# Performance work log

Measured on AMD Instinct MI355X. Metric: run time of the kernel, lower is better.

The kernel has to match this reference:

```python
import jax, jax.numpy as jnp
import numpy as np

T, B, NA = 32, 32, 5          # timesteps, envs, actions
HID, FEAT = 256, 512          # lstm hidden, cnn features
IN_DIM = FEAT + NA            # lstm input size (517)
FLAT = 64 * 7 * 7             # cnn flatten size (3136)


def _conv(x, w, b, s):
    # x: NCHW, w: OIHW, VALID padding, stride s
    y = jax.lax.conv_general_dilated(x, w, (s, s), 'VALID',
                                     dimension_numbers=('NCHW', 'OIHW', 'NCHW'))
    return y + b[None, :, None, None]


def setup_inputs() -> dict:
    key = jax.random.key(0)
    ks = jax.random.split(key, 24)
    p = lambda k, shape: (jax.random.normal(k, shape, jnp.float32) * 0.05)
    return {
        'image': jax.random.uniform(ks[0], (T * B, 3, 84, 84), jnp.float32) * 255.0,
        'last_action': jax.random.randint(ks[1], (T * B,), 0, NA),
        'done': jax.random.bernoulli(ks[2], 0.05, (T * B,)).astype(jnp.float32),
        'h0': jnp.zeros((B, HID), jnp.float32),
        'c0': jnp.zeros((B, HID), jnp.float32),
        # NatureCNN params
        'W1': p(ks[3], (32, 3, 8, 8)), 'b1': jnp.zeros((32,), jnp.float32),
        'W2': p(ks[4], (64, 32, 4, 4)), 'b2': jnp.zeros((64,), jnp.float32),
        'W3': p(ks[5], (64, 64, 3, 3)), 'b3': jnp.zeros((64,), jnp.float32),
        'Wfc': p(ks[6], (FEAT, FLAT)), 'bfc': jnp.zeros((FEAT,), jnp.float32),
        # LSTM params (torch gate order i,f,g,o)
        'W_ih': p(ks[7], (4 * HID, IN_DIM)), 'W_hh': p(ks[8], (4 * HID, HID)),
        'b_ih': jnp.zeros((4 * HID,), jnp.float32), 'b_hh': jnp.zeros((4 * HID,), jnp.float32),
        # policy MLP (hidden 64, tanh)
        'Wp1': p(ks[9], (64, HID)), 'bp1': jnp.zeros((64,), jnp.float32),
        'Wp2': p(ks[10], (NA, 64)) * 0.01, 'bp2': jnp.zeros((NA,), jnp.float32),
        # value MLP
        'Wv1': p(ks[11], (64, HID)), 'bv1': jnp.zeros((64,), jnp.float32),
        'Wv2': p(ks[12], (1, 64)), 'bv2': jnp.zeros((1,), jnp.float32),
    }


def reference(image, last_action, done, h0, c0,
              W1, b1, W2, b2, W3, b3, Wfc, bfc,
              W_ih, W_hh, b_ih, b_hh,
              Wp1, bp1, Wp2, bp2, Wv1, bv1, Wv2, bv2):
    # --- extract: NatureCNN + one-hot(last_action) ---
    x = image / 255.0
    x = jax.nn.relu(_conv(x, W1, b1, 4))   # (TB,32,20,20)
    x = jax.nn.relu(_conv(x, W2, b2, 2))   # (TB,64,9,9)
    x = jax.nn.relu(_conv(x, W3, b3, 1))   # (TB,64,7,7)
    x = x.reshape(x.shape[0], -1)
    feat = jax.nn.relu(x @ Wfc.T + bfc)    # (TB,512)
    oh = jax.nn.one_hot(last_action, NA, dtype=feat.dtype)
    xs = jnp.concatenate([feat, oh], axis=1).reshape(T, B, IN_DIM)
    ds = done.reshape(T, B)

    # --- remember: done-masked LSTM recurrence (torch gate order i,f,g,o) ---
    def step(carry, inp):
        h, c = carry
        xt, dt = inp
        m = (1.0 - dt)[:, None]
        h = h * m
        c = c * m
        g = xt @ W_ih.T + b_ih + h @ W_hh.T + b_hh   # (B, 4*HID)
        i, f, gg, o = jnp.split(g, 4, axis=1)
        c = jax.nn.sigmoid(f) * c + jax.nn.sigmoid(i) * jnp.tanh(gg)
        h = jax.nn.sigmoid(o) * jnp.tanh(c)
        return (h, c), h

    (hT, cT), hs = jax.lax.scan(step, (h0, c0), (xs, ds))
    h = hs.reshape(T * B, HID)

    # --- heads ---
    logits = jnp.tanh(h @ Wp1.T + bp1) @ Wp2.T + bp2   # (TB, NA)
    v = jnp.tanh(h @ Wv1.T + bv1) @ Wv2.T + bv2        # (TB, 1)
    return logits, v, hT, cT
```

## Files before the change

kernel.cpp:

```cpp
#include <hip/hip_runtime.h>
#include <math.h>

typedef float  f4v __attribute__((ext_vector_type(4)));
typedef short  s8v __attribute__((ext_vector_type(8)));
typedef int    i4v __attribute__((ext_vector_type(4)));

__device__ __forceinline__ float sigm(float x) { return 1.f / (1.f + expf(-x)); }
__device__ __forceinline__ unsigned short f2bf(float f) {
    unsigned int u = __float_as_uint(f);
    return (unsigned short)((u + 0x7FFF + ((u >> 16) & 1)) >> 16);
}
__device__ __forceinline__ unsigned int cvt2(float lo, float hi) {
    unsigned int r;
    asm("v_cvt_pk_bf16_f32 %0, %1, %2" : "=v"(r) : "v"(lo), "v"(hi));
    return r;
}
__device__ __forceinline__ s8v pack8(float4 a, float4 b) {
    union { unsigned int u[4]; s8v v; } r;
    r.u[0] = cvt2(a.x, a.y); r.u[1] = cvt2(a.z, a.w);
    r.u[2] = cvt2(b.x, b.y); r.u[3] = cvt2(b.z, b.w);
    return r.v;
}

__global__ __launch_bounds__(256) void k_amax(const float* __restrict__ Whh,
                                              unsigned int* __restrict__ amax_bits) {
    int i = blockIdx.x * 256 + threadIdx.x;
    float v = fabsf(Whh[i]);
#pragma unroll
    for (int o = 1; o < 64; o <<= 1) v = fmaxf(v, __shfl_xor(v, o));
    if ((threadIdx.x & 63) == 0) atomicMax(amax_bits, __float_as_uint(v));
}

__global__ __launch_bounds__(256) void k_prep(const float* __restrict__ W2, const float* __restrict__ W3,
                                              const float* __restrict__ Wfc, const float* __restrict__ Wih,
                                              const float* __restrict__ W1, const float* __restrict__ Whh,
                                              const unsigned int* __restrict__ amax_bits,
                                              unsigned short* __restrict__ W2p, unsigned short* __restrict__ W3p,
                                              unsigned short* __restrict__ Wfcp, unsigned short* __restrict__ Wihp,
                                              unsigned short* __restrict__ W1p, signed char* __restrict__ Wq) {
    int i = blockIdx.x * 256 + threadIdx.x;
    if (i < 32768) {
        int co = i >> 9, k = i & 511, t = k >> 5, ci = k & 31, ky = t >> 2, kx = t & 3;
        W2p[i] = f2bf(W2[co * 512 + ci * 16 + ky * 4 + kx]);
    } else if (i < 69632) {
        int j = i - 32768;
        int co = j / 576, k = j - co * 576, t = k >> 6, ci = k & 63;
        int ky = t / 3, kx = t - ky * 3;
        W3p[j] = f2bf(W3[((co * 64 + ci) * 3 + ky) * 3 + kx]);
    } else if (i < 1675264) {
        int j = i - 69632;
        Wfcp[j] = f2bf(Wfc[j]);
    } else if (i < 2199552) {
        int j = i - 1675264;
        int n = j >> 9, k = j & 511;
        Wihp[j] = f2bf(Wih[n * 517 + k]);
    } else if (i < 2205696) {
        int j = i - 2199552;
        W1p[j] = f2bf(W1[j] * (1.f / 255.f));
    } else if (i < 2467840) {
        int j = i - 2205696;
        float amax = __uint_as_float(amax_bits[0]);
        float s = 127.f / amax;
        int qv = (int)rintf(Whh[j] * s);
        qv = qv > 127 ? 127 : (qv < -127 ? -127 : qv);
        Wq[j] = (signed char)qv;
    }
}

__global__ __launch_bounds__(256) void k_conv1(const float* __restrict__ img,
                                               const unsigned short* __restrict__ Bw,
                                               const float* __restrict__ bias,
                                               unsigned short* __restrict__ out) {
    __shared__ unsigned short c1s[32][132];
    int lane = threadIdx.x & 63, w = threadIdx.x >> 6;
    int l15 = lane & 15, q = lane >> 4;
    int m0 = blockIdx.x * 128;
    const float* Ap[2];
#pragma unroll
    for (int mf = 0; mf < 2; ++mf) {
        int m = m0 + w * 32 + mf * 16 + l15;
        int im = m / 400, p = m - im * 400;
        int oy = p / 20, ox = p - oy * 20;
        Ap[mf] = img + im * 21168 + oy * 336 + ox * 4;
    }
    const unsigned short* Bp0 = Bw + l15 * 192 + q * 8;
    const unsigned short* Bp1 = Bw + (16 + l15) * 192 + q * 8;
    s8v bf0[6], bf1[6];
#pragma unroll
    for (int ks = 0; ks < 6; ++ks) {
        bf0[ks] = *(const s8v*)(Bp0 + ks * 32);
        bf1[ks] = *(const s8v*)(Bp1 + ks * 32);
    }
    int roffs[6];
#pragma unroll
    for (int ks = 0; ks < 6; ++ks) {
        int k0 = ks * 32 + q * 8;
        int c = k0 >> 6, ky = (k0 >> 3) & 7;
        roffs[ks] = c * 7056 + ky * 84;
    }
    f4v acc[4];
#pragma unroll
    for (int i = 0; i < 4; ++i) acc[i] = (f4v){0.f, 0.f, 0.f, 0.f};
#pragma unroll
    for (int ks = 0; ks < 6; ++ks) {
#pragma unroll
        for (int mf = 0; mf < 2; ++mf) {
            float4 a0 = *(const float4*)(Ap[mf] + roffs[ks]);
            float4 a1 = *(const float4*)(Ap[mf] + roffs[ks] + 4);
            s8v ua = pack8(a0, a1);
            acc[mf * 2 + 0] = __builtin_amdgcn_mfma_f32_16x16x32_bf16(ua, bf0[ks], acc[mf * 2 + 0], 0, 0, 0);
            acc[mf * 2 + 1] = __builtin_amdgcn_mfma_f32_16x16x32_bf16(ua, bf1[ks], acc[mf * 2 + 1], 0, 0, 0);
        }
    }
#pragma unroll
    for (int nf = 0; nf < 2; ++nf) {
        int n = nf * 16 + l15;
        float b = bias[n];
#pragma unroll
        for (int mf = 0; mf < 2; ++mf) {
            int ml = w * 32 + mf * 16 + q * 4;
#pragma unroll
            for (int r = 0; r < 4; r += 2) {
                float v0 = acc[mf * 2 + nf][r] + b;     v0 = v0 > 0.f ? v0 : 0.f;
                float v1 = acc[mf * 2 + nf][r + 1] + b; v1 = v1 > 0.f ? v1 : 0.f;
                *(unsigned int*)&c1s[n][ml + r] = cvt2(v0, v1);
            }
        }
    }
    __syncthreads();
#pragma unroll
    for (int seg = 0; seg < 16; ++seg) {
        int flat = seg * 256 + threadIdx.x;
        int n = flat >> 7, ml = flat & 127;
        int m = m0 + ml;
        int im = m / 400, p = m - im * 400;
        out[(im * 32 + n) * 400 + p] = c1s[n][ml];
    }
}

__global__ __launch_bounds__(256, 2) void k_conv2(const unsigned short* __restrict__ A,
                                                  const unsigned short* __restrict__ Bw,
                                                  const float* __restrict__ bias,
                                                  unsigned short* __restrict__ out) {
    __shared__ unsigned short sA[800 * 32];
    __shared__ unsigned short c2s[64][196];
    int tid = threadIdx.x;
    int lane = tid & 63, w = tid >> 6;
    int l15 = lane & 15, q = lane >> 4;
    int img0 = blockIdx.x * 2;
    char* sAb = (char*)sA;
    const s8v* srcv = (const s8v*)(A + img0 * 12800);
    for (int wi = tid; wi < 3200; wi += 256) {
        s8v v = srcv[wi];
        int f = wi * 8;
        int im = f / 12800, r = f - im * 12800, ci = r / 400, p = r - ci * 400;
#pragma unroll
        for (int j = 0; j < 8; ++j) {
            int R = im * 400 + p + j;
            int Rl = (R >> 1) + (R & 1) * 400;
            int by = (Rl * 32 + ci) * 2 ^ ((Rl & 7) << 4);
            *(unsigned short*)(sAb + by) = (unsigned short)v[j];
        }
    }
    __syncthreads();
    int Rb[3];
#pragma unroll
    for (int mf = 0; mf < 3; ++mf) {
        int t = w * 3 + mf;
        int im = t / 6;
        int pp = (t - im * 6) * 16 + l15;
        int px = pp > 80 ? 80 : pp;
        int oy = px / 9, ox = px - oy * 9;
        Rb[mf] = im * 400 + oy * 40 + ox * 2;
    }
    const unsigned short* Bp0 = Bw + l15 * 512 + q * 8;
    const unsigned short* Bp1 = Bw + (16 + l15) * 512 + q * 8;
    const unsigned short* Bp2 = Bw + (32 + l15) * 512 + q * 8;
    const unsigned short* Bp3 = Bw + (48 + l15) * 512 + q * 8;
    f4v acc[3][4];
#pragma unroll
    for (int i = 0; i < 3; ++i)
#pragma unroll
        for (int j = 0; j < 4; ++j) acc[i][j] = (f4v){0.f, 0.f, 0.f, 0.f};
#pragma unroll
    for (int s = 0; s < 16; ++s) {
        const int ky = s >> 2, kx = s & 3;
        const int d = ky * 20 + kx;
        s8v a[3];
#pragma unroll
        for (int mf = 0; mf < 3; ++mf) {
            int R = Rb[mf] + d;
            int Rl = (R >> 1) + (R & 1) * 400;
            int by = (Rl * 64 + q * 16) ^ ((Rl & 7) << 4);
            a[mf] = *(const s8v*)(sAb + by);
        }
        s8v b0 = *(const s8v*)(Bp0 + s * 32);
        s8v b1 = *(const s8v*)(Bp1 + s * 32);
        s8v b2 = *(const s8v*)(Bp2 + s * 32);
        s8v b3 = *(const s8v*)(Bp3 + s * 32);
#pragma unroll
        for (int mf = 0; mf < 3; ++mf) {
            acc[mf][0] = __builtin_amdgcn_mfma_f32_16x16x32_bf16(a[mf], b0, acc[mf][0], 0, 0, 0);
            acc[mf][1] = __builtin_amdgcn_mfma_f32_16x16x32_bf16(a[mf], b1, acc[mf][1], 0, 0, 0);
            acc[mf][2] = __builtin_amdgcn_mfma_f32_16x16x32_bf16(a[mf], b2, acc[mf][2], 0, 0, 0);
            acc[mf][3] = __builtin_amdgcn_mfma_f32_16x16x32_bf16(a[mf], b3, acc[mf][3], 0, 0, 0);
        }
    }
#pragma unroll
    for (int nf = 0; nf < 4; ++nf) {
        int co = nf * 16 + l15;
        float b = bias[co];
#pragma unroll
        for (int mf = 0; mf < 3; ++mf) {
            int rr = (w * 3 + mf) * 16 + q * 4;
#pragma unroll
            for (int r = 0; r < 4; r += 2) {
                float v0 = acc[mf][nf][r] + b;     v0 = v0 > 0.f ? v0 : 0.f;
                float v1 = acc[mf][nf][r + 1] + b; v1 = v1 > 0.f ? v1 : 0.f;
                *(unsigned int*)&c2s[co][rr + r] = cvt2(v0, v1);
            }
        }
    }
    __syncthreads();
    for (int idx = tid; idx < 10368; idx += 256) {
        int im = idx / 5184, r2 = idx - im * 5184, co = r2 / 81, p = r2 - co * 81;
        out[(img0 + im) * 5184 + r2] = c2s[co][im * 96 + p];
    }
}

__global__ __launch_bounds__(256, 2) void k_conv3(const unsigned short* __restrict__ A,
                                                  const unsigned short* __restrict__ Bw,
                                                  const float* __restrict__ bias,
                                                  unsigned short* __restrict__ out) {
    __shared__ unsigned short sA[162 * 64];
    __shared__ unsigned short c3s[64][132];
    int tid = threadIdx.x;
    int lane = tid & 63, w = tid >> 6;
    int l15 = lane & 15, q = lane >> 4;
    int img0 = blockIdx.x * 2;
    char* sAb = (char*)sA;
    const s8v* srcv = (const s8v*)(A + img0 * 5184);
    for (int wi = tid; wi < 1296; wi += 256) {
        s8v v = srcv[wi];
        int f = wi * 8;
#pragma unroll
        for (int j = 0; j < 8; ++j) {
            int fe = f + j;
            int im = fe / 5184, r = fe - im * 5184, ci = r / 81, p = r - ci * 81;
            int R = im * 81 + p;
            int by = (R * 64 + ci) * 2 ^ ((R & 7) << 4);
            *(unsigned short*)(sAb + by) = (unsigned short)v[j];
        }
    }
    __syncthreads();
    int Rb[2];
#pragma unroll
    for (int mf = 0; mf < 2; ++mf) {
        int t = w * 2 + mf;
        int im = t >> 2;
        int pp = (t & 3) * 16 + l15;
        int px = pp > 48 ? 48 : pp;
        int oy = px / 7, ox = px - oy * 7;
        Rb[mf] = im * 81 + oy * 9 + ox;
    }
    const unsigned short* Bp0 = Bw + l15 * 576 + q * 8;
    const unsigned short* Bp1 = Bw + (16 + l15) * 576 + q * 8;
    const unsigned short* Bp2 = Bw + (32 + l15) * 576 + q * 8;
    const unsigned short* Bp3 = Bw + (48 + l15) * 576 + q * 8;
    f4v acc[2][4];
#pragma unroll
    for (int i = 0; i < 2; ++i)
#pragma unroll
        for (int j = 0; j < 4; ++j) acc[i][j] = (f4v){0.f, 0.f, 0.f, 0.f};
#pragma unroll
    for (int s = 0; s < 18; ++s) {
        const int tap = s >> 1, cb2 = (s & 1) * 64;
        const int ky = tap / 3, kx = tap - ky * 3;
        const int d = ky * 9 + kx;
        s8v a0, a1;
        {
            int R = Rb[0] + d;
            int by = (R * 128 + cb2 + q * 16) ^ ((R & 7) << 4);
            a0 = *(const s8v*)(sAb + by);
        }
        {
            int R = Rb[1] + d;
            int by = (R * 128 + cb2 + q * 16) ^ ((R & 7) << 4);
            a1 = *(const s8v*)(sAb + by);
        }
        s8v b0 = *(const s8v*)(Bp0 + s * 32);
        s8v b1 = *(const s8v*)(Bp1 + s * 32);
        s8v b2 = *(const s8v*)(Bp2 + s * 32);
        s8v b3 = *(const s8v*)(Bp3 + s * 32);
        acc[0][0] = __builtin_amdgcn_mfma_f32_16x16x32_bf16(a0, b0, acc[0][0], 0, 0, 0);
        acc[0][1] = __builtin_amdgcn_mfma_f32_16x16x32_bf16(a0, b1, acc[0][1], 0, 0, 0);
        acc[0][2] = __builtin_amdgcn_mfma_f32_16x16x32_bf16(a0, b2, acc[0][2], 0, 0, 0);
        acc[0][3] = __builtin_amdgcn_mfma_f32_16x16x32_bf16(a0, b3, acc[0][3], 0, 0, 0);
        acc[1][0] = __builtin_amdgcn_mfma_f32_16x16x32_bf16(a1, b0, acc[1][0], 0, 0, 0);
        acc[1][1] = __builtin_amdgcn_mfma_f32_16x16x32_bf16(a1, b1, acc[1][1], 0, 0, 0);
        acc[1][2] = __builtin_amdgcn_mfma_f32_16x16x32_bf16(a1, b2, acc[1][2], 0, 0, 0);
        acc[1][3] = __builtin_amdgcn_mfma_f32_16x16x32_bf16(a1, b3, acc[1][3], 0, 0, 0);
    }
#pragma unroll
    for (int nf = 0; nf < 4; ++nf) {
        int co = nf * 16 + l15;
        float b = bias[co];
#pragma unroll
        for (int mf = 0; mf < 2; ++mf) {
            int rr = (w * 2 + mf) * 16 + q * 4;
#pragma unroll
            for (int r = 0; r < 4; r += 2) {
                float v0 = acc[mf][nf][r] + b;     v0 = v0 > 0.f ? v0 : 0.f;
                float v1 = acc[mf][nf][r + 1] + b; v1 = v1 > 0.f ? v1 : 0.f;
                *(unsigned int*)&c3s[co][rr + r] = cvt2(v0, v1);
            }
        }
    }
    __syncthreads();
    for (int idx = tid; idx < 6272; idx += 256) {
        int im = idx / 3136, r2 = idx - im * 3136, co = r2 / 49, p = r2 - co * 49;
        out[(img0 + im) * 3136 + r2] = c3s[co][im * 64 + p];
    }
}

__global__ __launch_bounds__(256) void k_fc(const unsigned short* __restrict__ A,
                                            const unsigned short* __restrict__ Bw,
                                            const float* __restrict__ bias,
                                            unsigned short* __restrict__ out) {
    int lane = threadIdx.x & 63, w = threadIdx.x >> 6;
    int l15 = lane & 15, q = lane >> 4;
    int m0 = blockIdx.x * 32 + (w & 1) * 16;
    int n0 = blockIdx.y * 64 + (w >> 1) * 32;
    const unsigned short* Ap = A + (m0 + l15) * 3136 + q * 8;
    const unsigned short* B0 = Bw + (n0 + l15) * 3136 + q * 8;
    const unsigned short* B1 = B0 + 16 * 3136;
    f4v acc0 = (f4v){0.f, 0.f, 0.f, 0.f}, acc1 = (f4v){0.f, 0.f, 0.f, 0.f};
    s8v av = *(const s8v*)Ap, b0 = *(const s8v*)B0, b1 = *(const s8v*)B1;
    for (int c = 0; c < 97; ++c) {
        Ap += 32; B0 += 32; B1 += 32;
        s8v nav = *(const s8v*)Ap, nb0 = *(const s8v*)B0, nb1 = *(const s8v*)B1;
        acc0 = __builtin_amdgcn_mfma_f32_16x16x32_bf16(av, b0, acc0, 0, 0, 0);
        acc1 = __builtin_amdgcn_mfma_f32_16x16x32_bf16(av, b1, acc1, 0, 0, 0);
        av = nav; b0 = nb0; b1 = nb1;
    }
    acc0 = __builtin_amdgcn_mfma_f32_16x16x32_bf16(av, b0, acc0, 0, 0, 0);
    acc1 = __builtin_amdgcn_mfma_f32_16x16x32_bf16(av, b1, acc1, 0, 0, 0);
    float bi0 = bias[n0 + l15], bi1 = bias[n0 + 16 + l15];
#pragma unroll
    for (int r = 0; r < 4; ++r) {
        int m = m0 + q * 4 + r;
        float v0 = acc0[r] + bi0; v0 = v0 > 0.f ? v0 : 0.f;
        float v1 = acc1[r] + bi1; v1 = v1 > 0.f ? v1 : 0.f;
        out[m * 512 + n0 + l15] = f2bf(v0);
        out[m * 512 + n0 + 16 + l15] = f2bf(v1);
    }
}

__global__ __launch_bounds__(256) void k_gx(const unsigned short* __restrict__ A,
                                            const unsigned short* __restrict__ Bw,
                                            const float* __restrict__ Wih,
                                            const float* __restrict__ bih,
                                            const float* __restrict__ bhh,
                                            const int* __restrict__ act,
                                            float* __restrict__ out) {
    int lane = threadIdx.x & 63, w = threadIdx.x >> 6;
    int l15 = lane & 15, q = lane >> 4;
    int m0 = blockIdx.x * 32 + (w & 1) * 16;
    int n0 = blockIdx.y * 64 + (w >> 1) * 32;
    const unsigned short* Ap = A + (m0 + l15) * 512 + q * 8;
    const unsigned short* B0 = Bw + (n0 + l15) * 512 + q * 8;
    const unsigned short* B1 = B0 + 16 * 512;
    f4v acc0 = (f4v){0.f, 0.f, 0.f, 0.f}, acc1 = (f4v){0.f, 0.f, 0.f, 0.f};
    for (int c = 0; c < 16; ++c) {
        s8v av = *(const s8v*)Ap;
        s8v b0 = *(const s8v*)B0;
        s8v b1 = *(const s8v*)B1;
        Ap += 32; B0 += 32; B1 += 32;
        acc0 = __builtin_amdgcn_mfma_f32_16x16x32_bf16(av, b0, acc0, 0, 0, 0);
        acc1 = __builtin_amdgcn_mfma_f32_16x16x32_bf16(av, b1, acc1, 0, 0, 0);
    }
    int na = n0 + l15, nb = n0 + 16 + l15;
    float ca = bih[na] + bhh[na], cb_ = bih[nb] + bhh[nb];
#pragma unroll
    for (int r = 0; r < 4; ++r) {
        int m = m0 + q * 4 + r;
        int a = act[m];
        out[m * 1024 + na] = acc0[r] + Wih[na * 517 + 512 + a] + ca;
        out[m * 1024 + nb] = acc1[r] + Wih[nb * 517 + 512 + a] + cb_;
    }
}

__global__ __launch_bounds__(1024) void k_lstm_all(const float* __restrict__ h0,
                                                   const float* __restrict__ c0,
                                                   const float* __restrict__ done,
                                                   const float* __restrict__ gx,
                                                   const signed char* __restrict__ Wq,
                                                   const unsigned int* __restrict__ amax_bits,
                                                   float* __restrict__ hs,
                                                   float* __restrict__ cb) {
    int b = blockIdx.x;
    int tid = threadIdx.x;
    int w = tid >> 6, lane = tid & 63;
    int l15 = lane & 15, q = lane >> 4;
    __shared__ float gbuf[1024];
    __shared__ float cst[256];
    __shared__ signed char hA[4][64][16];

    i4v wfr[4][4];
    const signed char* wb = Wq + (w * 64 + l15) * 256 + q * 16;
#pragma unroll
    for (int s = 0; s < 4; ++s)
#pragma unroll
        for (int kf = 0; kf < 4; ++kf)
            wfr[s][kf] = *(const i4v*)(wb + s * 16 * 256 + kf * 64);
    float sw = __uint_as_float(amax_bits[0]) * (1.f / (127.f * 127.f));

    ((int*)hA)[tid] = 0;
    __syncthreads();
    if (tid < 256) {
        int u = tid;
        cst[u] = c0[b * 256 + u];
        float m0v = 1.f - done[b];
        float hv = h0[b * 256 + u] * m0v;
        hv = hv > 1.f ? 1.f : (hv < -1.f ? -1.f : hv);
        hA[u >> 6][((u >> 4) & 3) * 16][u & 15] = (signed char)(int)rintf(hv * 127.f);
    }
    __syncthreads();

    for (int t = 0; t < 32; ++t) {
        float gxi = 0.f, gxf = 0.f, gxg = 0.f, gxo = 0.f, dcur = 0.f, dnxt = 0.f;
        if (tid < 256) {
            const float* gr = gx + (t * 32 + b) * 1024;
            gxi = gr[tid]; gxf = gr[256 + tid]; gxg = gr[512 + tid]; gxo = gr[768 + tid];
            dcur = done[t * 32 + b];
            dnxt = (t < 31) ? done[(t + 1) * 32 + b] : 1.f;
        }
        i4v acc[4];
#pragma unroll
        for (int s = 0; s < 4; ++s) acc[s] = (i4v){0, 0, 0, 0};
#pragma unroll
        for (int kf = 0; kf < 4; ++kf) {
            i4v a = *(const i4v*)&hA[kf][lane][0];
#pragma unroll
            for (int s = 0; s < 4; ++s)
                acc[s] = __builtin_amdgcn_mfma_i32_16x16x64_i8(a, wfr[s][kf], acc[s], 0, 0, 0);
        }
        if (q == 0) {
#pragma unroll
            for (int s = 0; s < 4; ++s)
                gbuf[w * 64 + s * 16 + l15] = (float)acc[s][0];
        }
        __syncthreads();
        if (tid < 256) {
            int u = tid;
            float gi = gbuf[u] * sw + gxi;
            float gf = gbuf[256 + u] * sw + gxf;
            float gg = gbuf[512 + u] * sw + gxg;
            float go = gbuf[768 + u] * sw + gxo;
            float cm = cst[u] * (1.f - dcur);
            float cn = sigm(gf) * cm + sigm(gi) * tanhf(gg);
            float hn = sigm(go) * tanhf(cn);
            cst[u] = cn;
            hs[t * 8192 + b * 256 + u] = hn;
            float hv = hn * (1.f - dnxt);
            hA[u >> 6][((u >> 4) & 3) * 16][u & 15] = (signed char)(int)rintf(hv * 127.f);
        }
        __syncthreads();
    }
    if (tid < 256) cb[b * 256 + tid] = cst[tid];
}

__global__ __launch_bounds__(256) void k_heads(const float* __restrict__ hs,
                                               const float* __restrict__ cb,
                                               const float* __restrict__ Wp1, const float* __restrict__ bp1,
                                               const float* __restrict__ Wp2, const float* __restrict__ bp2,
                                               const float* __restrict__ Wv1, const float* __restrict__ bv1,
                                               const float* __restrict__ Wv2, const float* __restrict__ bv2,
                                               float* __restrict__ out) {
    int lane = threadIdx.x & 63;
    int m = blockIdx.x * 4 + (threadIdx.x >> 6);
    const float4* hv = (const float4*)(hs + m * 256);
    const float4* wp = (const float4*)(Wp1 + lane * 256);
    const float4* wq = (const float4*)(Wv1 + lane * 256);
    float ap = 0.f, av = 0.f;
#pragma unroll 8
    for (int k = 0; k < 64; ++k) {
        float4 h4 = hv[k];
        float4 p4 = wp[k];
        float4 q4 = wq[k];
        ap += h4.x * p4.x + h4.y * p4.y + h4.z * p4.z + h4.w * p4.w;
        av += h4.x * q4.x + h4.y * q4.y + h4.z * q4.z + h4.w * q4.w;
    }
    float hp = tanhf(ap + bp1[lane]);
    float hq = tanhf(av + bv1[lane]);
#pragma unroll
    for (int j = 0; j < 5; ++j) {
        float s = hp * Wp2[j * 64 + lane];
        s += __shfl_xor(s, 1); s += __shfl_xor(s, 2); s += __shfl_xor(s, 4);
        s += __shfl_xor(s, 8); s += __shfl_xor(s, 16); s += __shfl_xor(s, 32);
        if (lane == 0) out[m * 5 + j] = s + bp2[j];
    }
    float s = hq * Wv2[lane];
    s += __shfl_xor(s, 1); s += __shfl_xor(s, 2); s += __shfl_xor(s, 4);
    s += __shfl_xor(s, 8); s += __shfl_xor(s, 16); s += __shfl_xor(s, 32);
    if (lane == 0) out[5120 + m] = s + bv2[0];

    int g = blockIdx.x * 256 + threadIdx.x;
    if (g < 8192) {
        out[6144 + g] = hs[31 * 8192 + g];
        out[6144 + 8192 + g] = cb[g];
    }
}

extern "C" void kernel_launch(void* const* d_in, const int* in_sizes, int n_in,
                              void* d_out, int out_size, void* d_ws, size_t ws_size,
                              hipStream_t stream) {
    const float* image = (const float*)d_in[0];
    const int*   act   = (const int*)d_in[1];
    const float* done  = (const float*)d_in[2];
    const float* h0    = (const float*)d_in[3];
    const float* c0    = (const float*)d_in[4];
    const float* W1    = (const float*)d_in[5];
    const float* b1    = (const float*)d_in[6];
    const float* W2    = (const float*)d_in[7];
    const float* b2    = (const float*)d_in[8];
    const float* W3    = (const float*)d_in[9];
    const float* b3    = (const float*)d_in[10];
    const float* Wfc   = (const float*)d_in[11];
    const float* bfc   = (const float*)d_in[12];
    const float* Wih   = (const float*)d_in[13];
    const float* Whh   = (const float*)d_in[14];
    const float* bih   = (const float*)d_in[15];
    const float* bhh   = (const float*)d_in[16];
    const float* Wp1   = (const float*)d_in[17];
    const float* bp1   = (const float*)d_in[18];
    const float* Wp2   = (const float*)d_in[19];
    const float* bp2   = (const float*)d_in[20];
    const float* Wv1   = (const float*)d_in[21];
    const float* bv1   = (const float*)d_in[22];
    const float* Wv2   = (const float*)d_in[23];
    const float* bv2   = (const float*)d_in[24];
    float* out = (float*)d_out;
    char* base = (char*)d_ws;

    unsigned short* a1   = (unsigned short*)(base);
    unsigned short* a2   = (unsigned short*)(base + 26214432);
    unsigned short* W2p  = (unsigned short*)(base + 36831328);
    unsigned short* W3p  = (unsigned short*)(base + 36896864);
    unsigned short* Wfcp = (unsigned short*)(base + 36970592);
    unsigned short* Wihp = (unsigned short*)(base + 40181856);
    unsigned short* W1p  = (unsigned short*)(base + 41230432);
    unsigned int*   amax = (unsigned int*)(base + 41242752);
    signed char*    Wq   = (signed char*)(base + 41242784);
    unsigned short* a3   = (unsigned short*)(base);
    unsigned short* feat = (unsigned short*)(base + 6422528);
    float* gx = (float*)(base + 7471104);
    float* hs = (float*)(base + 11665408);
    float* cb = (float*)(base + 12713984);

    hipMemsetAsync(amax, 0, 4, stream);
    k_amax<<<1024, 256, 0, stream>>>(Whh, amax);
    k_prep<<<9640, 256, 0, stream>>>(W2, W3, Wfc, Wih, W1, Whh, amax, W2p, W3p, Wfcp, Wihp, W1p, Wq);
    k_conv1<<<3200, 256, 0, stream>>>(image, W1p, b1, a1);
    k_conv2<<<512, 256, 0, stream>>>(a1, W2p, b2, a2);
    k_conv3<<<512, 256, 0, stream>>>(a2, W3p, b3, a3);
    k_fc<<<dim3(32, 8), 256, 0, stream>>>(a3, Wfcp, bfc, feat);
    k_gx<<<dim3(32, 16), 256, 0, stream>>>(feat, Wihp, Wih, bih, bhh, act, gx);
    k_lstm_all<<<32, 1024, 0, stream>>>(h0, c0, done, gx, Wq, amax, hs, cb);
    k_heads<<<256, 256, 0, stream>>>(hs, cb, Wp1, bp1, Wp2, bp2, Wv1, bv1, Wv2, bv2, out);
}
```

Baseline: 431.9 us.

## Stage whole image in LDS as bf16 for conv1, one block per image

conv1 now assigns one 512-thread block per image. Each block first converts the whole 3x84x84 fp32 image to bf16 in shared memory, then the MFMA A-fragments are read from LDS rather than as strided global float4 loads. Because stride-4 windows of size 8 overlap, each image pixel is now fetched from global memory about once instead of several times. The output tile reuses the same LDS buffer and is written out with coalesced 32-bit stores per image. The cost is about 42 KB of LDS per block, which limits occupancy, and only 25 of 32 wave-tile slots do work.

```diff
diff --git a/kernel.cpp b/kernel.cpp
--- a/kernel.cpp
+++ b/kernel.cpp
@@ -14,12 +14,6 @@
     unsigned int r;
     asm("v_cvt_pk_bf16_f32 %0, %1, %2" : "=v"(r) : "v"(lo), "v"(hi));
     return r;
-}
-__device__ __forceinline__ s8v pack8(float4 a, float4 b) {
-    union { unsigned int u[4]; s8v v; } r;
-    r.u[0] = cvt2(a.x, a.y); r.u[1] = cvt2(a.z, a.w);
-    r.u[2] = cvt2(b.x, b.y); r.u[3] = cvt2(b.z, b.w);
-    return r.v;
 }
 
 __global__ __launch_bounds__(256) void k_amax(const float* __restrict__ Whh,
@@ -67,22 +61,23 @@
     }
 }
 
-__global__ __launch_bounds__(256) void k_conv1(const float* __restrict__ img,
+__global__ __launch_bounds__(512) void k_conv1(const float* __restrict__ img,
                                                const unsigned short* __restrict__ Bw,
                                                const float* __restrict__ bias,
                                                unsigned short* __restrict__ out) {
-    __shared__ unsigned short c1s[32][132];
-    int lane = threadIdx.x & 63, w = threadIdx.x >> 6;
+    __shared__ unsigned short sImg[21168];
+    int tid = threadIdx.x;
+    int lane = tid & 63, w = tid >> 6;
     int l15 = lane & 15, q = lane >> 4;
-    int m0 = blockIdx.x * 128;
-    const float* Ap[2];
-#pragma unroll
-    for (int mf = 0; mf < 2; ++mf) {
-        int m = m0 + w * 32 + mf * 16 + l15;
-        int im = m / 400, p = m - im * 400;
-        int oy = p / 20, ox = p - oy * 20;
-        Ap[mf] = img + im * 21168 + oy * 336 + ox * 4;
-    }
+    int im = blockIdx.x;
+    const float4* srcv = (const float4*)(img + im * 21168);
+    unsigned int* sW = (unsigned int*)sImg;
+    for (int wi = tid; wi < 5292; wi += 512) {
+        float4 v = srcv[wi];
+        sW[wi * 2]     = cvt2(v.x, v.y);
+        sW[wi * 2 + 1] = cvt2(v.z, v.w);
+    }
+    __syncthreads();
     const unsigned short* Bp0 = Bw + l15 * 192 + q * 8;
     const unsigned short* Bp1 = Bw + (16 + l15) * 192 + q * 8;
     s8v bf0[6], bf1[6];
@@ -91,50 +86,55 @@
         bf0[ks] = *(const s8v*)(Bp0 + ks * 32);
         bf1[ks] = *(const s8v*)(Bp1 + ks * 32);
     }
-    int roffs[6];
+    int woff[6];
 #pragma unroll
     for (int ks = 0; ks < 6; ++ks) {
         int k0 = ks * 32 + q * 8;
         int c = k0 >> 6, ky = (k0 >> 3) & 7;
-        roffs[ks] = c * 7056 + ky * 84;
-    }
-    f4v acc[4];
-#pragma unroll
-    for (int i = 0; i < 4; ++i) acc[i] = (f4v){0.f, 0.f, 0.f, 0.f};
-#pragma unroll
-    for (int ks = 0; ks < 6; ++ks) {
-#pragma unroll
-        for (int mf = 0; mf < 2; ++mf) {
-            float4 a0 = *(const float4*)(Ap[mf] + roffs[ks]);
-            float4 a1 = *(const float4*)(Ap[mf] + roffs[ks] + 4);
-            s8v ua = pack8(a0, a1);
-            acc[mf * 2 + 0] = __builtin_amdgcn_mfma_f32_16x16x32_bf16(ua, bf0[ks], acc[mf * 2 + 0], 0, 0, 0);
-            acc[mf * 2 + 1] = __builtin_amdgcn_mfma_f32_16x16x32_bf16(ua, bf1[ks], acc[mf * 2 + 1], 0, 0, 0);
-        }
-    }
-#pragma unroll
-    for (int nf = 0; nf < 2; ++nf) {
-        int n = nf * 16 + l15;
-        float b = bias[n];
-#pragma unroll
-        for (int mf = 0; mf < 2; ++mf) {
-            int ml = w * 32 + mf * 16 + q * 4;
+        woff[ks] = c * 7056 + ky * 84;
+    }
+    f4v acc[4][2];
+#pragma unroll
+    for (int i = 0; i < 4; ++i) { acc[i][0] = (f4v){0.f,0.f,0.f,0.f}; acc[i][1] = (f4v){0.f,0.f,0.f,0.f}; }
+#pragma unroll
+    for (int tt = 0; tt < 4; ++tt) {
+        int t = w + tt * 8;
+        if (t < 25) {
+            int pA = t * 16 + l15;
+            int oy = pA / 20, ox = pA - oy * 20;
+            const unsigned short* ab = sImg + oy * 336 + ox * 4;
+#pragma unroll
+            for (int ks = 0; ks < 6; ++ks) {
+                s8v a = *(const s8v*)(ab + woff[ks]);
+                acc[tt][0] = __builtin_amdgcn_mfma_f32_16x16x32_bf16(a, bf0[ks], acc[tt][0], 0, 0, 0);
+                acc[tt][1] = __builtin_amdgcn_mfma_f32_16x16x32_bf16(a, bf1[ks], acc[tt][1], 0, 0, 0);
+            }
+        }
+    }
+    __syncthreads();
+    float b0v = bias[l15], b1v = bias[16 + l15];
+#pragma unroll
+    for (int tt = 0; tt < 4; ++tt) {
+        int t = w + tt * 8;
+        if (t < 25) {
+            int pc = t * 16 + q * 4;
 #pragma unroll
             for (int r = 0; r < 4; r += 2) {
-                float v0 = acc[mf * 2 + nf][r] + b;     v0 = v0 > 0.f ? v0 : 0.f;
-                float v1 = acc[mf * 2 + nf][r + 1] + b; v1 = v1 > 0.f ? v1 : 0.f;
-                *(unsigned int*)&c1s[n][ml + r] = cvt2(v0, v1);
+                float v0 = acc[tt][0][r] + b0v;     v0 = v0 > 0.f ? v0 : 0.f;
+                float v1 = acc[tt][0][r + 1] + b0v; v1 = v1 > 0.f ? v1 : 0.f;
+                *(unsigned int*)&sImg[l15 * 404 + pc + r] = cvt2(v0, v1);
+                float u0 = acc[tt][1][r] + b1v;     u0 = u0 > 0.f ? u0 : 0.f;
+                float u1 = acc[tt][1][r + 1] + b1v; u1 = u1 > 0.f ? u1 : 0.f;
+                *(unsigned int*)&sImg[(16 + l15) * 404 + pc + r] = cvt2(u0, u1);
             }
         }
     }
     __syncthreads();
-#pragma unroll
-    for (int seg = 0; seg < 16; ++seg) {
-        int flat = seg * 256 + threadIdx.x;
-        int n = flat >> 7, ml = flat & 127;
-        int m = m0 + ml;
-        int im = m / 400, p = m - im * 400;
-        out[(im * 32 + n) * 400 + p] = c1s[n][ml];
+    const unsigned int* cw = (const unsigned int*)sImg;
+    unsigned int* ow = (unsigned int*)(out + im * 12800);
+    for (int i = tid; i < 6400; i += 512) {
+        int n = i / 200, rem = i - n * 200;
+        ow[i] = cw[n * 202 + rem];
     }
 }
 
@@ -561,7 +561,7 @@
     hipMemsetAsync(amax, 0, 4, stream);
     k_amax<<<1024, 256, 0, stream>>>(Whh, amax);
     k_prep<<<9640, 256, 0, stream>>>(W2, W3, Wfc, Wih, W1, Whh, amax, W2p, W3p, Wfcp, Wihp, W1p, Wq);
-    k_conv1<<<3200, 256, 0, stream>>>(image, W1p, b1, a1);
+    k_conv1<<<1024, 512, 0, stream>>>(image, W1p, b1, a1);
     k_conv2<<<512, 256, 0, stream>>>(a1, W2p, b2, a2);
     k_conv3<<<512, 256, 0, stream>>>(a2, W3p, b3, a3);
     k_fc<<<dim3(32, 8), 256, 0, stream>>>(a3, Wfcp, bfc, feat);
```

Result: no change. 428.8 us (-0.7%).
